# Optimization experiments

Hardware: AMD Instinct MI355X
Metric: run time of the kernel (lower is better)

## Reference

```python
import jax, jax.numpy as jnp
import numpy as np

NODE_F = 8      # node_features
HID = 128       # hidden_dim
HEADS = 8       # nn.MultiheadAttention num_heads
OUT = 256       # output_dim
MAX_ATOMS = 4096  # max_pocket_atoms
NEIGHBOR_RADIUS = 3.0   # _compute_surface_scores neighbor_radius


def setup_inputs() -> dict:
    key = jax.random.key(0)
    ks = jax.random.split(key, 16)
    N, M = 16384, 32
    x = jax.random.normal(ks[0], (N, NODE_F), dtype=jnp.float32)
    pos = jax.random.normal(ks[1], (N, 3), dtype=jnp.float32) * 10.0
    ligand_pos = jax.random.normal(ks[2], (M, 3), dtype=jnp.float32) * 3.0

    def lin(k, fan_in, fan_out):
        return jax.random.normal(k, (fan_in, fan_out), dtype=jnp.float32) / np.sqrt(fan_in)

    return {
        'x': x, 'pos': pos, 'ligand_pos': ligand_pos,
        'W_node': lin(ks[3], NODE_F, HID), 'b_node': jnp.zeros((HID,), jnp.float32),
        'Wq': lin(ks[4], HID, HID), 'bq': jnp.zeros((HID,), jnp.float32),
        'Wk': lin(ks[5], HID, HID), 'bk': jnp.zeros((HID,), jnp.float32),
        'Wv': lin(ks[6], HID, HID), 'bv': jnp.zeros((HID,), jnp.float32),
        'Wo': lin(ks[7], HID, HID), 'bo': jnp.zeros((HID,), jnp.float32),
        'W1': lin(ks[8], HID, OUT), 'b1': jnp.zeros((OUT,), jnp.float32),
        'W2': lin(ks[9], OUT, OUT), 'b2': jnp.zeros((OUT,), jnp.float32),
    }


def _select_binding_site(pos, ligand_pos, k):
    # select_by_binding_site_proximity: distance-to-ligand-center + surface scores, topk
    lig_center = jnp.mean(ligand_pos, axis=0)                       # [3]
    d_lig = jnp.linalg.norm(pos - lig_center, axis=1)               # [N]
    # _compute_surface_scores: cdist(pos,pos) < 3.0, count neighbors (minus self)
    sq = jnp.sum(pos * pos, axis=1)                                 # [N]
    d2 = sq[:, None] + sq[None, :] - 2.0 * (pos @ pos.T)            # [N,N] squared distances
    neighbor_counts = jnp.sum(d2 < NEIGHBOR_RADIUS ** 2, axis=1) - 1
    surface = 1.0 / (neighbor_counts.astype(jnp.float32) + 1.0)
    scores = 1.0 / (1.0 + d_lig / 5.0) + 0.5 * surface
    _, idx = jax.lax.top_k(scores, k)                               # largest=True
    return idx


def reference(x, pos, ligand_pos, W_node, b_node, Wq, bq, Wk, bk, Wv, bv, Wo, bo, W1, b1, W2, b2):
    # N > max_pocket_atoms -> smart selection (adaptive with ligand_pos => binding_site)
    idx = _select_binding_site(pos, ligand_pos, MAX_ATOMS)
    xs = x[idx]                                                     # [K, NODE_F]

    # node embedding (E3 net call fails in the original -> h = node_embedding(x))
    h = xs @ W_node + b_node                                        # [K, HID]

    # MultiheadAttention over the single (batch=None) sequence, eval mode (no dropout)
    K = MAX_ATOMS
    dh = HID // HEADS
    q = (h @ Wq + bq).reshape(K, HEADS, dh).transpose(1, 0, 2)      # [H,K,dh]
    k_ = (h @ Wk + bk).reshape(K, HEADS, dh).transpose(1, 0, 2)
    v = (h @ Wv + bv).reshape(K, HEADS, dh).transpose(1, 0, 2)
    attn = jax.nn.softmax(jnp.einsum('hqd,hkd->hqk', q, k_) / np.sqrt(dh), axis=-1)
    av = jnp.einsum('hqk,hkd->hqd', attn, v).transpose(1, 0, 2).reshape(K, HID)
    h_att = av @ Wo + bo                                            # [K, HID]

    # global mean pool + output projection (Linear-ReLU-Linear)
    pooled = jnp.mean(h_att, axis=0)                                # [HID]
    out = jax.nn.relu(pooled @ W1 + b1) @ W2 + b2                   # [OUT]
    return out
```

## Files before the change

### kernel.cpp

```cpp
#include <hip/hip_runtime.h>
#include <cstdint>
#include <cstddef>

#define NPTS 16384
#define KSEL 4096
#define HIDDEN 128
#define NHEADS 8
#define DHEAD 16
#define OUTD 256
#define NSLICE 4
#define FCAP 131072
#define LCAP 2048
#define TAU 0.2f

typedef __attribute__((ext_vector_type(8))) short bf16x8;
typedef __attribute__((ext_vector_type(4))) float f32x4;

#if defined(__has_builtin)
#if __has_builtin(__builtin_amdgcn_exp2f)
#define E2(x) __builtin_amdgcn_exp2f(x)
#endif
#endif
#ifndef E2
#define E2(x) exp2f(x)
#endif

constexpr size_t OFF_PA    = 1024;
constexpr size_t OFF_PB    = OFF_PA  + (size_t)NPTS*32;
constexpr size_t OFF_SQ    = OFF_PB  + (size_t)NPTS*32;
constexpr size_t OFF_DL    = OFF_SQ  + (size_t)NPTS*4;
constexpr size_t OFF_CNT   = OFF_DL  + (size_t)NPTS*4;
constexpr size_t OFF_NFLAG = OFF_CNT + (size_t)NPTS*4;
constexpr size_t OFF_FLG   = OFF_NFLAG + 1024;
constexpr size_t OFF_SEL   = OFF_FLG + (size_t)FCAP*4;
constexpr size_t SZ_PK     = (size_t)NHEADS*KSEL*32*2;
constexpr size_t OFF_QPK   = OFF_SEL + (size_t)KSEL*4;
constexpr size_t OFF_KPK   = OFF_QPK + SZ_PK;
constexpr size_t OFF_V     = OFF_KPK + SZ_PK;
constexpr size_t OFF_LP    = OFF_V  + (size_t)KSEL*HIDDEN*4;
constexpr size_t OFF_RL    = OFF_LP + (size_t)NHEADS*KSEL*NSLICE*4;
constexpr size_t OFF_WP    = OFF_RL + (size_t)NHEADS*KSEL*4;
constexpr size_t OFF_PAV   = OFF_WP + (size_t)NHEADS*KSEL*NSLICE*4;

__device__ __forceinline__ unsigned short f2bf(float f) {
    union { float f; unsigned u; } v; v.f = f;
    unsigned r = v.u + 0x7fffu + ((v.u >> 16) & 1u);
    return (unsigned short)(r >> 16);
}
__device__ __forceinline__ float bf2f(unsigned short h) {
    union { unsigned u; float f; } v; v.u = ((unsigned)h) << 16;
    return v.f;
}

__global__ void __launch_bounds__(256) k_prep(const float* __restrict__ pos, const float* __restrict__ lig, int M,
                       unsigned short* __restrict__ pa, unsigned short* __restrict__ pb,
                       float* __restrict__ sq, float* __restrict__ dl) {
    __shared__ float ls[128];
    __shared__ float ctr[3];
    int tid = threadIdx.x;
    for (int i = tid; i < 3 * M; i += 256) ls[i] = lig[i];
    __syncthreads();
    if (tid < 3) {
        float s = 0.f;
        for (int i = 0; i < M; i++) s += ls[i * 3 + tid];
        ctr[tid] = s / (float)M;
    }
    __syncthreads();
    int i = blockIdx.x * 256 + tid;
    float x = pos[i*3+0], y = pos[i*3+1], z = pos[i*3+2];
    float s = (x*x + y*y) + z*z;
    sq[i] = s;
    float dx = x - ctr[0], dy = y - ctr[1], dz = z - ctr[2];
    dl[i] = sqrtf((dx*dx + dy*dy) + dz*dz);
    unsigned short xh = f2bf(x); float xr = bf2f(xh); float xl = x - xr;
    unsigned short yh = f2bf(y); float yr = bf2f(yh); float yl = y - yr;
    unsigned short zh = f2bf(z); float zr = bf2f(zh); float zl = z - zr;
    unsigned short xlb = f2bf(xl), ylb = f2bf(yl), zlb = f2bf(zl);
    unsigned short xhA = f2bf(-2.f*xr), xlA = f2bf(-2.f*xl);
    unsigned short yhA = f2bf(-2.f*yr), ylA = f2bf(-2.f*yl);
    unsigned short zhA = f2bf(-2.f*zr), zlA = f2bf(-2.f*zl);
    unsigned short sih = f2bf(s);
    unsigned short sil = f2bf(s - bf2f(sih));
    unsigned short one = f2bf(1.0f);
    union { unsigned short s[16]; float4 f[2]; } A, B;
    A.s[0]=xhA; A.s[1]=xhA; A.s[2]=xlA;
    A.s[3]=yhA; A.s[4]=yhA; A.s[5]=ylA;
    A.s[6]=zhA; A.s[7]=zhA; A.s[8]=zlA;
    A.s[9]=xlA; A.s[10]=ylA; A.s[11]=zlA;
    A.s[12]=sih; A.s[13]=sil; A.s[14]=one; A.s[15]=one;
    B.s[0]=xh;  B.s[1]=xlb;  B.s[2]=xh;
    B.s[3]=yh;  B.s[4]=ylb;  B.s[5]=yh;
    B.s[6]=zh;  B.s[7]=zlb;  B.s[8]=zh;
    B.s[9]=xlb; B.s[10]=ylb; B.s[11]=zlb;
    B.s[12]=one; B.s[13]=one; B.s[14]=sih; B.s[15]=sil;
    float4* pad = (float4*)(pa + (size_t)i * 16);
    pad[0] = A.f[0]; pad[1] = A.f[1];
    float4* pbd = (float4*)(pb + (size_t)i * 16);
    pbd[0] = B.f[0]; pbd[1] = B.f[1];
}

__global__ void __launch_bounds__(256) k_neighbor(
        const unsigned short* __restrict__ pa, const unsigned short* __restrict__ pb,
        int* __restrict__ cnt, unsigned int* __restrict__ flg, unsigned int* __restrict__ nflag) {
    int s = blockIdx.x, ch = blockIdx.y;
    int jb0 = ch * 2048;
    if (jb0 + 2048 <= s * 64) return;
    __shared__ unsigned short bs[256 * 24];
    __shared__ int colcnt[2048];
    __shared__ unsigned int fbuf[LCAP];
    __shared__ unsigned int fcnt, fbase;
    int tid = threadIdx.x;
    for (int i = tid; i < 2048; i += 256) colcnt[i] = 0;
    if (tid == 0) fcnt = 0;
    int lane = tid & 63, w = tid >> 6;
    int n = lane & 15, g = lane >> 4;
    int i0 = s * 64 + w * 16;
    bf16x8 afrag = {0,0,0,0,0,0,0,0};
    if (g < 2) afrag = *(const bf16x8*)(pa + (size_t)(i0 + n) * 16 + g * 8);
    int irow = i0 + g * 4;
    int boff = (g < 2) ? g * 8 : 0;
    int c0 = 0, c1 = 0, c2 = 0, c3 = 0;
    for (int sub = 0; sub < 8; sub++) {
        int jb = jb0 + sub * 256;
        if (jb + 256 <= s * 64) continue;
        __syncthreads();
        {
            const float4* src = (const float4*)(pb + (size_t)(jb + tid) * 16);
            float4 v0 = src[0], v1 = src[1];
            float4* dst = (float4*)&bs[tid * 24];
            dst[0] = v0; dst[1] = v1;
        }
        __syncthreads();
        for (int t = 0; t < 16; t++) {
            int jt = jb + t * 16;
            if (jt < i0) continue;
            bool sym = (jt > i0);
            bf16x8 bfrag = *(const bf16x8*)&bs[(t * 16 + n) * 24 + boff];
            f32x4 c = {0.f, 0.f, 0.f, 0.f};
            c = __builtin_amdgcn_mfma_f32_16x16x32_bf16(afrag, bfrag, c, 0, 0, 0);
            bool a0 = c[0] < (9.0f - TAU), a1 = c[1] < (9.0f - TAU);
            bool a2 = c[2] < (9.0f - TAU), a3 = c[3] < (9.0f - TAU);
            bool f0 = (c[0] < 9.0f + TAU) && !a0, f1 = (c[1] < 9.0f + TAU) && !a1;
            bool f2 = (c[2] < 9.0f + TAU) && !a2, f3 = (c[3] < 9.0f + TAU) && !a3;
            c0 += a0; c1 += a1; c2 += a2; c3 += a3;
            if (sym) {
                int sl = (int)a0 + (int)a1 + (int)a2 + (int)a3;
                sl += __shfl_xor(sl, 16);
                sl += __shfl_xor(sl, 32);
                if (g == 0 && sl != 0) atomicAdd(&colcnt[jt - jb0 + n], sl);
            }
            if (f0 | f1 | f2 | f3) {
                unsigned sb = sym ? (1u << 28) : 0u;
                int j = jt + n;
                if (f0) { unsigned xx = atomicAdd(&fcnt, 1u); if (xx < LCAP) fbuf[xx] = sb | ((unsigned)(irow+0) << 14) | (unsigned)j; }
                if (f1) { unsigned xx = atomicAdd(&fcnt, 1u); if (xx < LCAP) fbuf[xx] = sb | ((unsigned)(irow+1) << 14) | (unsigned)j; }
                if (f2) { unsigned xx = atomicAdd(&fcnt, 1u); if (xx < LCAP) fbuf[xx] = sb | ((unsigned)(irow+2) << 14) | (unsigned)j; }
                if (f3) { unsigned xx = atomicAdd(&fcnt, 1u); if (xx < LCAP) fbuf[xx] = sb | ((unsigned)(irow+3) << 14) | (unsigned)j; }
            }
        }
    }
    #pragma unroll
    for (int m = 1; m < 16; m <<= 1) {
        c0 += __shfl_xor(c0, m); c1 += __shfl_xor(c1, m);
        c2 += __shfl_xor(c2, m); c3 += __shfl_xor(c3, m);
    }
    if (n == 0) {
        if (c0) atomicAdd(&cnt[irow+0], c0);
        if (c1) atomicAdd(&cnt[irow+1], c1);
        if (c2) atomicAdd(&cnt[irow+2], c2);
        if (c3) atomicAdd(&cnt[irow+3], c3);
    }
    __syncthreads();
    for (int i = tid; i < 2048; i += 256) {
        int v = colcnt[i];
        if (v) atomicAdd(&cnt[jb0 + i], v);
    }
    if (tid == 0) {
        unsigned cf = fcnt; if (cf > LCAP) cf = LCAP;
        fcnt = cf;
        fbase = atomicAdd(nflag, cf);
    }
    __syncthreads();
    unsigned cf = fcnt, fb = fbase;
    for (unsigned xx = tid; xx < cf; xx += 256) {
        unsigned di = fb + xx;
        if (di < FCAP) flg[di] = fbuf[xx];
    }
}

__global__ void __launch_bounds__(256) k_fixup(const float* __restrict__ pos, const float* __restrict__ sq,
        const unsigned int* __restrict__ flg, const unsigned int* __restrict__ nflag,
        int* __restrict__ cnt) {
    int nf = (int)*nflag; if (nf > FCAP) nf = FCAP;
    for (int idx = blockIdx.x * 256 + threadIdx.x; idx < nf; idx += gridDim.x * 256) {
        unsigned pr = flg[idx];
        int i = (int)((pr >> 14) & 16383u), j = (int)(pr & 16383u);
        float xi = pos[i*3+0], yi = pos[i*3+1], zi = pos[i*3+2];
        float xj = pos[j*3+0], yj = pos[j*3+1], zj = pos[j*3+2];
        float dot = fmaf(xi, xj, fmaf(yi, yj, zi * zj));
        float d2 = (sq[i] + sq[j]) - 2.0f * dot;
        if (d2 < 9.0f) {
            atomicAdd(&cnt[i], 1);
            if (pr & (1u << 28)) atomicAdd(&cnt[j], 1);
        }
    }
}

__global__ void __launch_bounds__(1024) k_select(const float* __restrict__ dl, const int* __restrict__ cnt,
                                                 int* __restrict__ sel) {
    __shared__ unsigned int sk[NPTS];
    __shared__ int hist[256];
    __shared__ int scan2[256];
    __shared__ unsigned int s_prefix;
    __shared__ int s_rem, s_eqtot, s_nout, s_digit, s_cgt;
    int tid = threadIdx.x;
    for (int i = tid; i < NPTS; i += 1024) {
        float score = 1.0f / (1.0f + dl[i] / 5.0f) + 0.5f * (1.0f / (float)cnt[i]);
        unsigned int u = __float_as_uint(score);
        sk[i] = u ^ ((u & 0x80000000u) ? 0xFFFFFFFFu : 0x80000000u);
    }
    if (tid == 0) { s_prefix = 0; s_rem = KSEL; s_nout = 0; s_eqtot = 0; }
    __syncthreads();
    for (int p = 0; p < 4; p++) {
        int sh = 24 - 8 * p;
        if (tid < 256) hist[tid] = 0;
        __syncthreads();
        unsigned int pref = s_prefix;
        int shp = (p == 0) ? 0 : (32 - 8 * p);
        for (int i = tid; i < NPTS; i += 1024) {
            unsigned int key = sk[i];
            bool m = (p == 0) || ((key >> shp) == pref);
            if (m) atomicAdd(&hist[(key >> sh) & 255], 1);
        }
        __syncthreads();
        if (tid < 256) scan2[tid] = hist[tid];
        __syncthreads();
        for (int off = 1; off < 256; off <<= 1) {
            int v = 0;
            if (tid < 256) { v = scan2[tid]; if (tid + off < 256) v += scan2[tid + off]; }
            __syncthreads();
            if (tid < 256) scan2[tid] = v;
            __syncthreads();
        }
        int rem = s_rem;
        if (tid < 256) {
            int hi = scan2[tid];
            int lo = hi - hist[tid];
            if (hi >= rem && lo < rem) { s_digit = tid; s_cgt = lo; }
        }
        __syncthreads();
        if (tid == 0) {
            s_prefix = (s_prefix << 8) | (unsigned int)s_digit;
            s_rem = rem - s_cgt;
            if (p == 3) s_eqtot = hist[s_digit];
        }
        __syncthreads();
    }
    unsigned int T = s_prefix;
    int need_eq = s_rem;
    for (int i = tid; i < NPTS; i += 1024)
        if (sk[i] > T) sel[atomicAdd(&s_nout, 1)] = i;
    __syncthreads();
    if (s_eqtot == need_eq) {
        for (int i = tid; i < NPTS; i += 1024)
            if (sk[i] == T) sel[atomicAdd(&s_nout, 1)] = i;
    } else {
        for (int i = tid; i < NPTS; i += 1024) {
            if (sk[i] == T) {
                int rank = 0;
                for (int j = 0; j < i; j++) rank += (sk[j] == T);
                if (rank < need_eq) sel[atomicAdd(&s_nout, 1)] = i;
            }
        }
    }
}

__device__ __forceinline__ void proj4(const float hs[4][HIDDEN], const float* __restrict__ W,
                                      float b, int d, float* acc) {
    #pragma unroll
    for (int r = 0; r < 4; r++) acc[r] = b;
    for (int c = 0; c < HIDDEN; c += 4) {
        float w0 = W[(c+0)*HIDDEN+d], w1 = W[(c+1)*HIDDEN+d], w2 = W[(c+2)*HIDDEN+d], w3 = W[(c+3)*HIDDEN+d];
        #pragma unroll
        for (int r = 0; r < 4; r++) {
            float4 h4 = *(const float4*)&hs[r][c];
            float a = acc[r];
            a = fmaf(h4.x, w0, a); a = fmaf(h4.y, w1, a); a = fmaf(h4.z, w2, a); a = fmaf(h4.w, w3, a);
            acc[r] = a;
        }
    }
}

__global__ void __launch_bounds__(128) k_qkv(const float* __restrict__ x, const int* __restrict__ sel,
        const float* __restrict__ Wn, const float* __restrict__ bn,
        const float* __restrict__ Wq, const float* __restrict__ bq,
        const float* __restrict__ Wk, const float* __restrict__ bk,
        const float* __restrict__ Wv, const float* __restrict__ bv,
        unsigned short* __restrict__ qpk, unsigned short* __restrict__ kpk,
        float* __restrict__ vg) {
    __shared__ float xs[4][8];
    __shared__ __align__(16) float hs[4][HIDDEN];
    int d = threadIdx.x;
    int r0 = blockIdx.x * 4;
    if (d < 32) { int rr = d >> 3, cc = d & 7; xs[rr][cc] = x[(size_t)sel[r0 + rr] * 8 + cc]; }
    __syncthreads();
    {
        float wn[8];
        #pragma unroll
        for (int c = 0; c < 8; c++) wn[c] = Wn[c * HIDDEN + d];
        float b = bn[d];
        #pragma unroll
        for (int r = 0; r < 4; r++) {
            float a = b;
            #pragma unroll
            for (int c = 0; c < 8; c++) a = fmaf(xs[r][c], wn[c], a);
            hs[r][d] = a;
        }
    }
    __syncthreads();
    int hh = d >> 4, dd = d & 15;
    float acc[4];
    proj4(hs, Wq, bq[d], d, acc);
    #pragma unroll
    for (int r = 0; r < 4; r++) {
        float val = acc[r] * 0.36067376022224085f;
        unsigned short hi = f2bf(val);
        unsigned short lo = f2bf(val - bf2f(hi));
        size_t idx = ((size_t)(hh * KSEL) + r0 + r) * 32 + dd;
        qpk[idx] = hi; qpk[idx + 16] = lo;
    }
    proj4(hs, Wk, bk[d], d, acc);
    #pragma unroll
    for (int r = 0; r < 4; r++) {
        float val = acc[r];
        unsigned short hi = f2bf(val);
        unsigned short lo = f2bf(val - bf2f(hi));
        size_t idx = ((size_t)(hh * KSEL) + r0 + r) * 32 + dd;
        kpk[idx] = hi; kpk[idx + 16] = lo;
    }
    proj4(hs, Wv, bv[d], d, acc);
    #pragma unroll
    for (int r = 0; r < 4; r++) vg[(size_t)(r0+r)*HIDDEN + d] = acc[r];
}

__global__ void __launch_bounds__(256) k_attn_l(
        const unsigned short* __restrict__ qpk, const unsigned short* __restrict__ kpk,
        float* __restrict__ lp) {
    __shared__ unsigned short smem[256 * 40];
    int tid = threadIdx.x;
    int ks = blockIdx.x, yg = blockIdx.y, h = blockIdx.z;
    size_t hb = (size_t)h * KSEL;
    int lane = tid & 63, w = tid >> 6;
    int n = lane & 15, g = lane >> 4;
    int q0w = yg * 64 + w * 16;
    bf16x8 afrag = *(const bf16x8*)(qpk + (hb + q0w + n) * 32 + g * 8);
    float l0 = 0.f, l1 = 0.f, l2 = 0.f, l3 = 0.f;
    int b1off = (g & 1) * 8;
    int b2off = 16 + g * 8;
    for (int kc = 0; kc < 4; kc++) {
        __syncthreads();
        {
            int krow = ks * 1024 + kc * 256 + tid;
            const float4* src = (const float4*)(kpk + (hb + krow) * 32);
            float4 a0 = src[0], a1 = src[1], a2 = src[2], a3 = src[3];
            float4* dst = (float4*)&smem[tid * 40];
            dst[0] = a0; dst[1] = a1; dst[2] = a2; dst[3] = a3;
        }
        __syncthreads();
        #pragma unroll 4
        for (int t = 0; t < 16; t++) {
            const unsigned short* rowp = &smem[(t * 16 + n) * 40];
            bf16x8 b1 = *(const bf16x8*)(rowp + b1off);
            bf16x8 b2 = {0,0,0,0,0,0,0,0};
            if (g < 2) b2 = *(const bf16x8*)(rowp + b2off);
            f32x4 c = {0.f, 0.f, 0.f, 0.f};
            c = __builtin_amdgcn_mfma_f32_16x16x32_bf16(afrag, b1, c, 0, 0, 0);
            c = __builtin_amdgcn_mfma_f32_16x16x32_bf16(afrag, b2, c, 0, 0, 0);
            l0 += E2(c[0]); l1 += E2(c[1]); l2 += E2(c[2]); l3 += E2(c[3]);
        }
    }
    #pragma unroll
    for (int m = 1; m < 16; m <<= 1) {
        l0 += __shfl_xor(l0, m); l1 += __shfl_xor(l1, m);
        l2 += __shfl_xor(l2, m); l3 += __shfl_xor(l3, m);
    }
    if (n == 0) {
        size_t base = (hb + q0w + g * 4) * NSLICE + ks;
        lp[base]            = l0; lp[base + NSLICE]     = l1;
        lp[base + 2*NSLICE] = l2; lp[base + 3*NSLICE]   = l3;
    }
}

__global__ void k_rl(const float* __restrict__ lp, float* __restrict__ rl) {
    int i = blockIdx.x * 256 + threadIdx.x;
    float4 p = ((const float4*)lp)[i];
    rl[i] = 1.0f / ((p.x + p.y) + (p.z + p.w));
}

__global__ void __launch_bounds__(256) k_attn_w(
        const unsigned short* __restrict__ qpk, const unsigned short* __restrict__ kpk,
        const float* __restrict__ rl, float* __restrict__ wp) {
    __shared__ unsigned short smem[256 * 40];
    __shared__ float rls[256];
    int tid = threadIdx.x;
    int qs = blockIdx.x, yg = blockIdx.y, h = blockIdx.z;
    size_t hb = (size_t)h * KSEL;
    int lane = tid & 63, w = tid >> 6;
    int n = lane & 15, g = lane >> 4;
    int j0w = yg * 64 + w * 16;
    bf16x8 afrag = *(const bf16x8*)(kpk + (hb + j0w + n) * 32 + g * 8);
    float w0 = 0.f, w1 = 0.f, w2 = 0.f, w3 = 0.f;
    int b1off = (g & 1) * 8;
    int b2off = 16 + g * 8;
    for (int qc = 0; qc < 4; qc++) {
        __syncthreads();
        {
            int qrow = qs * 1024 + qc * 256 + tid;
            const float4* src = (const float4*)(qpk + (hb + qrow) * 32);
            float4 a0 = src[0], a1 = src[1], a2 = src[2], a3 = src[3];
            float4* dst = (float4*)&smem[tid * 40];
            dst[0] = a0; dst[1] = a1; dst[2] = a2; dst[3] = a3;
            rls[tid] = rl[hb + qrow];
        }
        __syncthreads();
        #pragma unroll 4
        for (int t = 0; t < 16; t++) {
            const unsigned short* rowp = &smem[(t * 16 + n) * 40];
            bf16x8 b1 = *(const bf16x8*)(rowp + b1off);
            bf16x8 b2 = {0,0,0,0,0,0,0,0};
            if (g < 2) b2 = *(const bf16x8*)(rowp + b2off);
            f32x4 c = {0.f, 0.f, 0.f, 0.f};
            c = __builtin_amdgcn_mfma_f32_16x16x32_bf16(afrag, b1, c, 0, 0, 0);
            c = __builtin_amdgcn_mfma_f32_16x16x32_bf16(afrag, b2, c, 0, 0, 0);
            float rv = rls[t * 16 + n];
            w0 = fmaf(E2(c[0]), rv, w0); w1 = fmaf(E2(c[1]), rv, w1);
            w2 = fmaf(E2(c[2]), rv, w2); w3 = fmaf(E2(c[3]), rv, w3);
        }
    }
    #pragma unroll
    for (int m = 1; m < 16; m <<= 1) {
        w0 += __shfl_xor(w0, m); w1 += __shfl_xor(w1, m);
        w2 += __shfl_xor(w2, m); w3 += __shfl_xor(w3, m);
    }
    if (n == 0) {
        size_t base = (hb + j0w + g * 4) * NSLICE + qs;
        wp[base]            = w0; wp[base + NSLICE]     = w1;
        wp[base + 2*NSLICE] = w2; wp[base + 3*NSLICE]   = w3;
    }
}

__global__ void __launch_bounds__(256) k_colsum(const float* __restrict__ wp, const float* __restrict__ vg,
                                                float* __restrict__ pav) {
    __shared__ float wl[NHEADS][128];
    __shared__ float red[128];
    int tid = threadIdx.x;
    int jb = blockIdx.x * 128;
    for (int i = tid; i < NHEADS * 128; i += 256) {
        int h = i >> 7, jl = i & 127;
        float4 p = ((const float4*)wp)[(size_t)h * KSEL + jb + jl];
        wl[h][jl] = (p.x + p.y) + (p.z + p.w);
    }
    __syncthreads();
    int d = tid & 127, g = tid >> 7;
    int h = d >> 4;
    float acc = 0.f;
    for (int jl = g * 64; jl < g * 64 + 64; jl++)
        acc = fmaf(wl[h][jl], vg[(size_t)(jb + jl) * HIDDEN + d], acc);
    if (g == 1) red[d] = acc;
    __syncthreads();
    if (g == 0) atomicAdd(&pav[d], (acc + red[d]) * (1.0f / (float)KSEL));
}

__global__ void __launch_bounds__(256) k_final(const float* __restrict__ pav,
        const float* __restrict__ Wo, const float* __restrict__ bo,
        const float* __restrict__ W1, const float* __restrict__ b1,
        const float* __restrict__ W2, const float* __restrict__ b2,
        float* __restrict__ out) {
    __shared__ float sp[HIDDEN];
    __shared__ float st[OUTD];
    int t = threadIdx.x;
    if (t < HIDDEN) {
        float a = bo[t];
        for (int c = 0; c < HIDDEN; c++) a = fmaf(pav[c], Wo[c * HIDDEN + t], a);
        sp[t] = a;
    }
    __syncthreads();
    {
        float a = b1[t];
        for (int c = 0; c < HIDDEN; c++) a = fmaf(sp[c], W1[c * OUTD + t], a);
        st[t] = fmaxf(a, 0.f);
    }
    __syncthreads();
    {
        float o = b2[t];
        for (int c = 0; c < OUTD; c++) o = fmaf(st[c], W2[c * OUTD + t], o);
        out[t] = o;
    }
}

extern "C" void kernel_launch(void* const* d_in, const int* in_sizes, int n_in,
                              void* d_out, int out_size, void* d_ws, size_t ws_size,
                              hipStream_t stream) {
    (void)n_in; (void)out_size; (void)ws_size;
    const float* x   = (const float*)d_in[0];
    const float* pos = (const float*)d_in[1];
    const float* lig = (const float*)d_in[2];
    const float* Wn  = (const float*)d_in[3];
    const float* bn  = (const float*)d_in[4];
    const float* Wq  = (const float*)d_in[5];
    const float* bq  = (const float*)d_in[6];
    const float* Wk  = (const float*)d_in[7];
    const float* bk  = (const float*)d_in[8];
    const float* Wv  = (const float*)d_in[9];
    const float* bv  = (const float*)d_in[10];
    const float* Wo  = (const float*)d_in[11];
    const float* bo  = (const float*)d_in[12];
    const float* W1  = (const float*)d_in[13];
    const float* b1  = (const float*)d_in[14];
    const float* W2  = (const float*)d_in[15];
    const float* b2  = (const float*)d_in[16];
    int M = in_sizes[2] / 3;

    char* ws = (char*)d_ws;
    unsigned short* pa  = (unsigned short*)(ws + OFF_PA);
    unsigned short* pb  = (unsigned short*)(ws + OFF_PB);
    float*          sq  = (float*)(ws + OFF_SQ);
    float*          dl  = (float*)(ws + OFF_DL);
    int*            cnt = (int*)  (ws + OFF_CNT);
    unsigned int*   nfl = (unsigned int*)(ws + OFF_NFLAG);
    unsigned int*   flg = (unsigned int*)(ws + OFF_FLG);
    int*            sel = (int*)  (ws + OFF_SEL);
    unsigned short* qpk = (unsigned short*)(ws + OFF_QPK);
    unsigned short* kpk = (unsigned short*)(ws + OFF_KPK);
    float*          vg  = (float*)(ws + OFF_V);
    float*          lp  = (float*)(ws + OFF_LP);
    float*          rl  = (float*)(ws + OFF_RL);
    float*          wp  = (float*)(ws + OFF_WP);
    float*          pav = (float*)(ws + OFF_PAV);

    hipMemsetAsync(ws + OFF_CNT, 0, (size_t)NPTS * 4 + 1024, stream);
    hipMemsetAsync(ws + OFF_PAV, 0, (size_t)HIDDEN * 4, stream);

    hipLaunchKernelGGL(k_prep,     dim3(64),       dim3(256),  0, stream, pos, lig, M, pa, pb, sq, dl);
    hipLaunchKernelGGL(k_neighbor, dim3(256, 8),   dim3(256),  0, stream, pa, pb, cnt, flg, nfl);
    hipLaunchKernelGGL(k_fixup,    dim3(32),       dim3(256),  0, stream, pos, sq, flg, nfl, cnt);
    hipLaunchKernelGGL(k_select,   dim3(1),        dim3(1024), 0, stream, dl, cnt, sel);
    hipLaunchKernelGGL(k_qkv,      dim3(KSEL/4),   dim3(128),  0, stream, x, sel, Wn, bn, Wq, bq, Wk, bk, Wv, bv, qpk, kpk, vg);
    hipLaunchKernelGGL(k_attn_l,   dim3(4, 64, 8), dim3(256),  0, stream, qpk, kpk, lp);
    hipLaunchKernelGGL(k_rl,       dim3(NHEADS*KSEL/256), dim3(256), 0, stream, lp, rl);
    hipLaunchKernelGGL(k_attn_w,   dim3(4, 64, 8), dim3(256),  0, stream, qpk, kpk, rl, wp);
    hipLaunchKernelGGL(k_colsum,   dim3(32),       dim3(256),  0, stream, wp, vg, pav);
    hipLaunchKernelGGL(k_final,    dim3(1),        dim3(256),  0, stream, pav, Wo, bo, W1, b1, W2, b2, (float*)d_out);
}
```

Baseline: 294.4 us.

## Compute full neighbor matrix with 32x32 MFMA instead of symmetric triangle

Rewrites the neighbor-count kernel to compute the full N×N distance matrix with 32x32x16 bf16 MFMA tiles, where each lane owns one row and accumulates its count in a register. This drops the upper-triangle symmetry bookkeeping, the column-count shared-memory atomics, and the per-tile symmetric flag. The intent is to remove atomic and branch overhead and use larger MFMA tiles, at the cost of doing roughly twice the pair evaluations. The fixup kernel now increments only the row index. Borderline pairs are still pushed to the flag buffer, roughly twice as many of them now, which raises the risk of LCAP/FCAP overflow.

```diff
diff --git a/kernel.cpp b/kernel.cpp
--- a/kernel.cpp
+++ b/kernel.cpp
@@ -15,6 +15,7 @@
 
 typedef __attribute__((ext_vector_type(8))) short bf16x8;
 typedef __attribute__((ext_vector_type(4))) float f32x4;
+typedef __attribute__((ext_vector_type(16))) float f32x16;
 
 #if defined(__has_builtin)
 #if __has_builtin(__builtin_amdgcn_exp2f)
@@ -102,79 +103,56 @@
 __global__ void __launch_bounds__(256) k_neighbor(
         const unsigned short* __restrict__ pa, const unsigned short* __restrict__ pb,
         int* __restrict__ cnt, unsigned int* __restrict__ flg, unsigned int* __restrict__ nflag) {
-    int s = blockIdx.x, ch = blockIdx.y;
-    int jb0 = ch * 2048;
-    if (jb0 + 2048 <= s * 64) return;
-    __shared__ unsigned short bs[256 * 24];
-    __shared__ int colcnt[2048];
+    __shared__ unsigned short js[256 * 24];
     __shared__ unsigned int fbuf[LCAP];
     __shared__ unsigned int fcnt, fbase;
     int tid = threadIdx.x;
-    for (int i = tid; i < 2048; i += 256) colcnt[i] = 0;
     if (tid == 0) fcnt = 0;
     int lane = tid & 63, w = tid >> 6;
-    int n = lane & 15, g = lane >> 4;
-    int i0 = s * 64 + w * 16;
-    bf16x8 afrag = {0,0,0,0,0,0,0,0};
-    if (g < 2) afrag = *(const bf16x8*)(pa + (size_t)(i0 + n) * 16 + g * 8);
-    int irow = i0 + g * 4;
-    int boff = (g < 2) ? g * 8 : 0;
-    int c0 = 0, c1 = 0, c2 = 0, c3 = 0;
-    for (int sub = 0; sub < 8; sub++) {
-        int jb = jb0 + sub * 256;
-        if (jb + 256 <= s * 64) continue;
+    int half = lane >> 5, il = lane & 31;
+    int i = blockIdx.x * 128 + w * 32 + il;
+    bf16x8 bfrag = *(const bf16x8*)(pb + (size_t)i * 16 + half * 8);
+    int jb0 = blockIdx.y * 2048;
+    int acc = 0;
+    for (int chv = 0; chv < 8; chv++) {
+        int jb = jb0 + chv * 256;
         __syncthreads();
         {
-            const float4* src = (const float4*)(pb + (size_t)(jb + tid) * 16);
+            const float4* src = (const float4*)(pa + (size_t)(jb + tid) * 16);
             float4 v0 = src[0], v1 = src[1];
-            float4* dst = (float4*)&bs[tid * 24];
+            float4* dst = (float4*)&js[tid * 24];
             dst[0] = v0; dst[1] = v1;
         }
         __syncthreads();
-        for (int t = 0; t < 16; t++) {
-            int jt = jb + t * 16;
-            if (jt < i0) continue;
-            bool sym = (jt > i0);
-            bf16x8 bfrag = *(const bf16x8*)&bs[(t * 16 + n) * 24 + boff];
-            f32x4 c = {0.f, 0.f, 0.f, 0.f};
-            c = __builtin_amdgcn_mfma_f32_16x16x32_bf16(afrag, bfrag, c, 0, 0, 0);
-            bool a0 = c[0] < (9.0f - TAU), a1 = c[1] < (9.0f - TAU);
-            bool a2 = c[2] < (9.0f - TAU), a3 = c[3] < (9.0f - TAU);
-            bool f0 = (c[0] < 9.0f + TAU) && !a0, f1 = (c[1] < 9.0f + TAU) && !a1;
-            bool f2 = (c[2] < 9.0f + TAU) && !a2, f3 = (c[3] < 9.0f + TAU) && !a3;
-            c0 += a0; c1 += a1; c2 += a2; c3 += a3;
-            if (sym) {
-                int sl = (int)a0 + (int)a1 + (int)a2 + (int)a3;
-                sl += __shfl_xor(sl, 16);
-                sl += __shfl_xor(sl, 32);
-                if (g == 0 && sl != 0) atomicAdd(&colcnt[jt - jb0 + n], sl);
+        #pragma unroll 2
+        for (int t = 0; t < 8; t++) {
+            bf16x8 afrag = *(const bf16x8*)&js[(t * 32 + il) * 24 + half * 8];
+            f32x16 c = {0.f,0.f,0.f,0.f,0.f,0.f,0.f,0.f,0.f,0.f,0.f,0.f,0.f,0.f,0.f,0.f};
+            c = __builtin_amdgcn_mfma_f32_32x32x16_bf16(afrag, bfrag, c, 0, 0, 0);
+            int cs = 0, cl = 0;
+            #pragma unroll
+            for (int r = 0; r < 16; r++) {
+                cs += (c[r] < 9.0f - TAU);
+                cl += (c[r] < 9.0f + TAU);
             }
-            if (f0 | f1 | f2 | f3) {
-                unsigned sb = sym ? (1u << 28) : 0u;
-                int j = jt + n;
-                if (f0) { unsigned xx = atomicAdd(&fcnt, 1u); if (xx < LCAP) fbuf[xx] = sb | ((unsigned)(irow+0) << 14) | (unsigned)j; }
-                if (f1) { unsigned xx = atomicAdd(&fcnt, 1u); if (xx < LCAP) fbuf[xx] = sb | ((unsigned)(irow+1) << 14) | (unsigned)j; }
-                if (f2) { unsigned xx = atomicAdd(&fcnt, 1u); if (xx < LCAP) fbuf[xx] = sb | ((unsigned)(irow+2) << 14) | (unsigned)j; }
-                if (f3) { unsigned xx = atomicAdd(&fcnt, 1u); if (xx < LCAP) fbuf[xx] = sb | ((unsigned)(irow+3) << 14) | (unsigned)j; }
+            acc += cs;
+            if (cl != cs) {
+                int jt = jb + t * 32;
+                #pragma unroll
+                for (int r = 0; r < 16; r++) {
+                    float d = c[r];
+                    if (d < 9.0f + TAU && d >= 9.0f - TAU) {
+                        int j = jt + (r & 3) + 8 * (r >> 2) + 4 * half;
+                        unsigned xx = atomicAdd(&fcnt, 1u);
+                        if (xx < LCAP) fbuf[xx] = ((unsigned)i << 14) | (unsigned)j;
+                    }
+                }
             }
         }
     }
-    #pragma unroll
-    for (int m = 1; m < 16; m <<= 1) {
-        c0 += __shfl_xor(c0, m); c1 += __shfl_xor(c1, m);
-        c2 += __shfl_xor(c2, m); c3 += __shfl_xor(c3, m);
-    }
-    if (n == 0) {
-        if (c0) atomicAdd(&cnt[irow+0], c0);
-        if (c1) atomicAdd(&cnt[irow+1], c1);
-        if (c2) atomicAdd(&cnt[irow+2], c2);
-        if (c3) atomicAdd(&cnt[irow+3], c3);
-    }
-    __syncthreads();
-    for (int i = tid; i < 2048; i += 256) {
-        int v = colcnt[i];
-        if (v) atomicAdd(&cnt[jb0 + i], v);
-    }
+    acc += __shfl_xor(acc, 32);
+    if (half == 0) atomicAdd(&cnt[i], acc);
+    __syncthreads();
     if (tid == 0) {
         unsigned cf = fcnt; if (cf > LCAP) cf = LCAP;
         fcnt = cf;
@@ -199,10 +177,7 @@
         float xj = pos[j*3+0], yj = pos[j*3+1], zj = pos[j*3+2];
         float dot = fmaf(xi, xj, fmaf(yi, yj, zi * zj));
         float d2 = (sq[i] + sq[j]) - 2.0f * dot;
-        if (d2 < 9.0f) {
-            atomicAdd(&cnt[i], 1);
-            if (pr & (1u << 28)) atomicAdd(&cnt[j], 1);
-        }
+        if (d2 < 9.0f) atomicAdd(&cnt[i], 1);
     }
 }
 
@@ -542,7 +517,7 @@
     hipMemsetAsync(ws + OFF_PAV, 0, (size_t)HIDDEN * 4, stream);
 
     hipLaunchKernelGGL(k_prep,     dim3(64),       dim3(256),  0, stream, pos, lig, M, pa, pb, sq, dl);
-    hipLaunchKernelGGL(k_neighbor, dim3(256, 8),   dim3(256),  0, stream, pa, pb, cnt, flg, nfl);
+    hipLaunchKernelGGL(k_neighbor, dim3(128, 8),   dim3(256),  0, stream, pa, pb, cnt, flg, nfl);
     hipLaunchKernelGGL(k_fixup,    dim3(32),       dim3(256),  0, stream, pos, sq, flg, nfl, cnt);
     hipLaunchKernelGGL(k_select,   dim3(1),        dim3(1024), 0, stream, dl, cnt, sel);
     hipLaunchKernelGGL(k_qkv,      dim3(KSEL/4),   dim3(128),  0, stream, x, sel, Wn, bn, Wq, bq, Wk, bk, Wv, bv, qpk, kpk, vg);
```

New measurement: 289.2 us. Within noise of the previous version (-1.8%).
